# Performance work log

Hardware: AMD Instinct MI355X
Metric: run time of the kernel (lower is better)

The kernel has to match this reference:

```python
import jax, jax.numpy as jnp
import numpy as np

B, C, H, W = 8, 512, 64, 64
C8 = C // 8


def setup_inputs() -> dict:
    key = jax.random.key(0)
    ks = jax.random.split(key, 9)
    s = 1.0 / np.sqrt(C)
    return {
        "view1": jax.random.normal(ks[0], (B, C, H, W), jnp.float32),
        "view2": jax.random.normal(ks[1], (B, C, H, W), jnp.float32),
        "Wq": jax.random.normal(ks[2], (C8, C), jnp.float32) * s,
        "bq": jax.random.normal(ks[3], (C8,), jnp.float32) * 0.01,
        "Wk": jax.random.normal(ks[4], (C8, C), jnp.float32) * s,
        "bk": jax.random.normal(ks[5], (C8,), jnp.float32) * 0.01,
        "Wv": jax.random.normal(ks[6], (C, C), jnp.float32) * s,
        "bv": jax.random.normal(ks[7], (C,), jnp.float32) * 0.01,
        "gamma": jnp.array([0.5], jnp.float32),  # nn.Parameter(zeros(1)) in torch; nonzero here for nontrivial output
    }


def reference(view1, view2, Wq, bq, Wk, bk, Wv, bv, gamma):
    b, c, h, w = view1.shape
    n = h * w
    # 1x1 convs == per-pixel linear over channel dim
    q = jnp.einsum("bchw,oc->bohw", view1, Wq) + bq[None, :, None, None]
    k = jnp.einsum("bchw,oc->bohw", view2, Wk) + bk[None, :, None, None]
    v = jnp.einsum("bchw,oc->bohw", view2, Wv) + bv[None, :, None, None]
    q = q.reshape(b, -1, n).transpose(0, 2, 1)  # (B, N, C/8)
    k = k.reshape(b, -1, n)                      # (B, C/8, N)
    v = v.reshape(b, c, n)                       # (B, C, N)
    # no scaling, matching the original module
    attn = jax.nn.softmax(jnp.einsum("bnd,bdm->bnm", q, k), axis=-1)  # (B, N, N)
    out = jnp.einsum("bcn,bmn->bcm", v, attn).reshape(b, c, h, w)
    return gamma[0] * out + view1
```

## Files before the change

### kernel.cpp

```cpp
#include <hip/hip_runtime.h>

#define NB 8
#define NC 512
#define NPIX 4096
#define LOG2E 1.44269504088896340736f
#define C0TERM 28.853900817779268f

typedef __attribute__((ext_vector_type(4))) float f32x4;
typedef __attribute__((ext_vector_type(8))) short bf16x8;
typedef __attribute__((ext_vector_type(4))) unsigned short u16x4;

static __device__ __forceinline__ short f2bf(float f){
    union { float f; unsigned u; } v; v.f = f;
    unsigned r = v.u + 0x7fffu + ((v.u >> 16) & 1u);
    return (short)(r >> 16);
}

static __device__ __forceinline__ void gload16(const void* g, void* l){
    __builtin_amdgcn_global_load_lds(
        (const __attribute__((address_space(1))) char*)g,
        (__attribute__((address_space(3))) char*)l, 16, 0, 0);
}

#define VW6 asm volatile("s_waitcnt vmcnt(6)" ::: "memory")
#define VW0 asm volatile("s_waitcnt vmcnt(0)" ::: "memory")
#define BAR __builtin_amdgcn_s_barrier()
#define SB0 __builtin_amdgcn_sched_barrier(0)

__global__ void k_wconv(const float* __restrict__ wq, const float* __restrict__ wk,
                        const float* __restrict__ wv,
                        short* __restrict__ wqb, short* __restrict__ wkb,
                        short* __restrict__ wvb){
    int i = blockIdx.x * 256 + threadIdx.x;
    if (i < 64*NC){ wqb[i] = f2bf(wq[i]); wkb[i] = f2bf(wk[i]); }
    if (i < NC*NC){ wvb[i] = f2bf(wv[i]); }
}

__global__ __launch_bounds__(256) void k_projq(const float* __restrict__ X,
                                               const short* __restrict__ W,
                                               const float* __restrict__ bias,
                                               short* __restrict__ out){
    const int b = blockIdx.y;
    const int wv = threadIdx.x >> 6;
    const int lane = threadIdx.x & 63;
    const int g = lane >> 4, c16 = lane & 15;
    const int n0w = blockIdx.x * 64 + wv * 16;
    const float* Xb = X + (size_t)b * NC * NPIX;

    f32x4 acc[4];
#pragma unroll
    for (int f = 0; f < 4; ++f) acc[f] = (f32x4){0.f,0.f,0.f,0.f};

    for (int c0 = 0; c0 < NC; c0 += 32){
        bf16x8 a;
#pragma unroll
        for (int j = 0; j < 8; ++j)
            a[j] = f2bf(Xb[(size_t)(c0 + 8*g + j) * NPIX + n0w + c16]);
#pragma unroll
        for (int f = 0; f < 4; ++f){
            bf16x8 bfr = *(const bf16x8*)(W + (size_t)(f*16 + c16) * NC + c0 + 8*g);
            acc[f] = __builtin_amdgcn_mfma_f32_16x16x32_bf16(a, bfr, acc[f], 0, 0, 0);
        }
    }
#pragma unroll
    for (int f = 0; f < 4; ++f){
        int o = f*16 + c16;
        float bo = bias[o];
#pragma unroll
        for (int i = 0; i < 4; ++i)
            out[((size_t)b*NPIX + n0w + 4*g + i)*64 + o] = f2bf(acc[f][i] + bo);
    }
}

__global__ __launch_bounds__(256) void k_trans(const float* __restrict__ X,
                                               short* __restrict__ Xt){
    __shared__ __align__(16) short T[64][72];
    const int n0 = blockIdx.x * 64;
    const int c0 = blockIdx.y * 64;
    const int b  = blockIdx.z;
    const int t  = threadIdx.x;
    {
        const int cl = t >> 2;
        const int nq = (t & 3) * 16;
        const float* src = X + ((size_t)b*NC + c0 + cl)*NPIX + n0 + nq;
#pragma unroll
        for (int q = 0; q < 4; ++q){
            f32x4 v = *(const f32x4*)(src + q*4);
#pragma unroll
            for (int i = 0; i < 4; ++i)
                T[nq + q*4 + i][cl] = f2bf(v[i]);
        }
    }
    __syncthreads();
    {
        const int n  = t >> 2;
        const int cs = (t & 3) * 16;
        short* dst = Xt + ((size_t)b*NPIX + n0 + n)*NC + c0 + cs;
        *(f32x4*)dst       = *(const f32x4*)&T[n][cs];
        *(f32x4*)(dst + 8) = *(const f32x4*)&T[n][cs + 8];
    }
}

__global__ __launch_bounds__(256) void k_projv(const short* __restrict__ Xt,
                                               const short* __restrict__ W,
                                               const float* __restrict__ bias,
                                               short* __restrict__ vout){
    const int o0 = blockIdx.x * 128;
    const int n0 = blockIdx.y * 128;
    const int b  = blockIdx.z;
    const int wv = threadIdx.x >> 6;
    const int lane = threadIdx.x & 63;
    const int g = lane >> 4, c16 = lane & 15;
    const int wo = wv & 1, wn = wv >> 1;

    const short* Xb = Xt + ((size_t)b*NPIX + n0 + wn*64)*NC;
    const short* Wb = W + (size_t)(o0 + wo*64)*NC;

    f32x4 acc[4][4];
#pragma unroll
    for (int nf = 0; nf < 4; ++nf)
#pragma unroll
        for (int of = 0; of < 4; ++of) acc[nf][of] = (f32x4){0.f,0.f,0.f,0.f};

    for (int c0 = 0; c0 < NC; c0 += 32){
        bf16x8 af[4], bf_[4];
#pragma unroll
        for (int f = 0; f < 4; ++f){
            af[f]  = *(const bf16x8*)(Xb + (size_t)(f*16 + c16)*NC + c0 + 8*g);
            bf_[f] = *(const bf16x8*)(Wb + (size_t)(f*16 + c16)*NC + c0 + 8*g);
        }
#pragma unroll
        for (int nf = 0; nf < 4; ++nf)
#pragma unroll
            for (int of = 0; of < 4; ++of)
                acc[nf][of] = __builtin_amdgcn_mfma_f32_16x16x32_bf16(af[nf], bf_[of], acc[nf][of], 0,0,0);
    }

#pragma unroll
    for (int of = 0; of < 4; ++of){
        int o = o0 + wo*64 + of*16 + c16;
        float bo = bias[o];
#pragma unroll
        for (int nf = 0; nf < 4; ++nf){
            int n = n0 + wn*64 + nf*16 + 4*g;
            u16x4 pk;
#pragma unroll
            for (int i = 0; i < 4; ++i) pk[i] = (unsigned short)f2bf(acc[nf][of][i] + bo);
            *(u16x4*)(vout + ((size_t)b*NC + o)*NPIX + n) = pk;
        }
    }
}

__global__ __launch_bounds__(256) void k_projk(const short* __restrict__ Xt,
                                               const short* __restrict__ W,
                                               const float* __restrict__ bias,
                                               short* __restrict__ kout){
    const int n0 = blockIdx.x * 256;
    const int b  = blockIdx.y;
    const int wv = threadIdx.x >> 6;
    const int lane = threadIdx.x & 63;
    const int g = lane >> 4, c16 = lane & 15;

    const short* Xb = Xt + ((size_t)b*NPIX + n0 + wv*64)*NC;

    f32x4 acc[4][4];
#pragma unroll
    for (int of = 0; of < 4; ++of)
#pragma unroll
        for (int nf = 0; nf < 4; ++nf) acc[of][nf] = (f32x4){0.f,0.f,0.f,0.f};

    for (int c0 = 0; c0 < NC; c0 += 32){
        bf16x8 af[4], bf_[4];
#pragma unroll
        for (int f = 0; f < 4; ++f){
            af[f]  = *(const bf16x8*)(W + (size_t)(f*16 + c16)*NC + c0 + 8*g);
            bf_[f] = *(const bf16x8*)(Xb + (size_t)(f*16 + c16)*NC + c0 + 8*g);
        }
#pragma unroll
        for (int of = 0; of < 4; ++of)
#pragma unroll
            for (int nf = 0; nf < 4; ++nf)
                acc[of][nf] = __builtin_amdgcn_mfma_f32_16x16x32_bf16(af[of], bf_[nf], acc[of][nf], 0,0,0);
    }

#pragma unroll
    for (int nf = 0; nf < 4; ++nf){
        int n = n0 + wv*64 + nf*16 + c16;
#pragma unroll
        for (int of = 0; of < 4; ++of){
            int o = of*16 + 4*g;
            u16x4 pk;
#pragma unroll
            for (int i = 0; i < 4; ++i) pk[i] = (unsigned short)f2bf(acc[of][nf][i] + bias[o+i]);
            *(u16x4*)(kout + ((size_t)b*NPIX + n)*64 + o) = pk;
        }
    }
}

__global__ __launch_bounds__(256) void k_projkv(const float* __restrict__ X,
                                                const short* __restrict__ Wv_,
                                                const float* __restrict__ bv_,
                                                const short* __restrict__ Wk_,
                                                const float* __restrict__ bk_,
                                                short* __restrict__ vout,
                                                short* __restrict__ kout){
    const int b = blockIdx.y;
    const int wv = threadIdx.x >> 6;
    const int lane = threadIdx.x & 63;
    const int g = lane >> 4, c16 = lane & 15;
    const int n0w = blockIdx.x * 32 + (wv & 1) * 16;
    const int oh = wv >> 1;
    const int o0v = oh * 256;
    const int o0k = oh * 32;
    const float* Xb = X + (size_t)b * NC * NPIX;

    f32x4 accv[16], acck[2];
#pragma unroll
    for (int f = 0; f < 16; ++f) accv[f] = (f32x4){0.f,0.f,0.f,0.f};
#pragma unroll
    for (int f = 0; f < 2;  ++f) acck[f] = (f32x4){0.f,0.f,0.f,0.f};

    for (int c0 = 0; c0 < NC; c0 += 32){
        bf16x8 a;
#pragma unroll
        for (int j = 0; j < 8; ++j)
            a[j] = f2bf(Xb[(size_t)(c0 + 8*g + j) * NPIX + n0w + c16]);
#pragma unroll
        for (int f = 0; f < 16; ++f){
            bf16x8 bfr = *(const bf16x8*)(Wv_ + (size_t)(o0v + f*16 + c16) * NC + c0 + 8*g);
            accv[f] = __builtin_amdgcn_mfma_f32_16x16x32_bf16(a, bfr, accv[f], 0, 0, 0);
        }
#pragma unroll
        for (int f = 0; f < 2; ++f){
            bf16x8 bfr = *(const bf16x8*)(Wk_ + (size_t)(o0k + f*16 + c16) * NC + c0 + 8*g);
            acck[f] = __builtin_amdgcn_mfma_f32_16x16x32_bf16(a, bfr, acck[f], 0, 0, 0);
        }
    }
#pragma unroll
    for (int f = 0; f < 16; ++f){
        int o = o0v + f*16 + c16;
        float bo = bv_[o];
        u16x4 pk;
#pragma unroll
        for (int i = 0; i < 4; ++i) pk[i] = (unsigned short)f2bf(accv[f][i] + bo);
        *(u16x4*)(vout + ((size_t)b*NC + o)*NPIX + n0w + 4*g) = pk;
    }
#pragma unroll
    for (int f = 0; f < 2; ++f){
        int o = o0k + f*16 + c16;
        float bo = bk_[o];
#pragma unroll
        for (int i = 0; i < 4; ++i)
            kout[((size_t)b*NPIX + n0w + 4*g + i)*64 + o] = f2bf(acck[f][i] + bo);
    }
}

__global__ __launch_bounds__(256) void k_qk(const short* __restrict__ qb,
                                            const short* __restrict__ kb,
                                            short* __restrict__ P,
                                            float* __restrict__ Lpart,
                                            int b0){
    __shared__ __align__(16) short Pt[64*256];
    const int m0 = blockIdx.x * 64;
    const int n0 = blockIdx.y * 256;
    const int bz = blockIdx.z;
    const int b  = b0 + bz;
    const int wv = threadIdx.x >> 6;
    const int lane = threadIdx.x & 63;
    const int g = lane >> 4, c16 = lane & 15;
    const int nsub = wv * 64;

    bf16x8 qf[4][2];
#pragma unroll
    for (int mf = 0; mf < 4; ++mf)
#pragma unroll
        for (int kk = 0; kk < 2; ++kk)
            qf[mf][kk] = *(const bf16x8*)(qb + ((size_t)b*NPIX + m0 + mf*16 + c16)*64 + kk*32 + 8*g);

    float lsum[4] = {0.f,0.f,0.f,0.f};
    char* Ptb = (char*)Pt;

#pragma unroll
    for (int nf = 0; nf < 4; ++nf){
        bf16x8 kf0 = *(const bf16x8*)(kb + ((size_t)b*NPIX + n0 + nsub + nf*16 + c16)*64 + 8*g);
        bf16x8 kf1 = *(const bf16x8*)(kb + ((size_t)b*NPIX + n0 + nsub + nf*16 + c16)*64 + 32 + 8*g);
#pragma unroll
        for (int mf = 0; mf < 4; ++mf){
            f32x4 s = (f32x4){0.f,0.f,0.f,0.f};
            s = __builtin_amdgcn_mfma_f32_16x16x32_bf16(kf0, qf[mf][0], s, 0,0,0);
            s = __builtin_amdgcn_mfma_f32_16x16x32_bf16(kf1, qf[mf][1], s, 0,0,0);
            u16x4 pk;
#pragma unroll
            for (int i = 0; i < 4; ++i){
                float p = exp2f(fmaf(s[i], LOG2E, -C0TERM));
                lsum[mf] += p;
                pk[i] = (unsigned short)f2bf(p);
            }
            int m = mf*16 + c16;
            int ncol = nsub + nf*16 + 4*g;
            *(u16x4*)(Ptb + m*512 + ((2*ncol) ^ ((m&7)<<4))) = pk;
        }
    }
    __syncthreads();

    {
        char* Pgb = (char*)(P + ((size_t)bz*NPIX + m0)*NPIX + n0);
        const int chunk = threadIdx.x & 31;
        const int row8  = threadIdx.x >> 5;
#pragma unroll
        for (int p = 0; p < 8; ++p){
            int row = p*8 + row8;
            f32x4 v = *(const f32x4*)(Ptb + row*512 + ((chunk*16) ^ ((row&7)<<4)));
            *(f32x4*)(Pgb + (size_t)row*(NPIX*2) + chunk*16) = v;
        }
    }

#pragma unroll
    for (int mf = 0; mf < 4; ++mf){
        lsum[mf] += __shfl_xor(lsum[mf], 16);
        lsum[mf] += __shfl_xor(lsum[mf], 32);
    }
    if (lane < 16){
        size_t base = ((size_t)bz*64 + blockIdx.y*4 + wv)*NPIX + m0 + lane;
#pragma unroll
        for (int mf = 0; mf < 4; ++mf)
            Lpart[base + mf*16] = lsum[mf];
    }
}

__global__ __launch_bounds__(256) void k_lred(const float* __restrict__ Lpart,
                                              const float* __restrict__ gamma,
                                              float* __restrict__ scale){
    int idx = blockIdx.x * 256 + threadIdx.x;
    int bz = idx >> 12, m = idx & 4095;
    float s = 0.f;
    for (int sl = 0; sl < 64; ++sl)
        s += Lpart[((size_t)bz*64 + sl)*NPIX + m];
    scale[idx] = gamma[0] / s;
}

__global__ __launch_bounds__(256) void k_pv(const short* __restrict__ vb,
                                            const short* __restrict__ P,
                                            const float* __restrict__ scale,
                                            const float* __restrict__ view1,
                                            float* __restrict__ out,
                                            int b0){
    __shared__ __align__(16) short At[2][128*64];
    __shared__ __align__(16) short Bt[2][64*64];
    const int p  = blockIdx.x + 4*blockIdx.y;
    const int mt = (p & 7) | ((p >> 5) << 3);
    const int ct = (p >> 3) & 3;
    const int c0 = ct * 128;
    const int m0 = mt * 64;
    const int bz = blockIdx.z;
    const int b  = b0 + bz;
    const int wv = threadIdx.x >> 6;
    const int lane = threadIdx.x & 63;
    const int g = lane >> 4, c16 = lane & 15;
    const int wc = wv & 1, wm = wv >> 1;
    const int lrow = lane >> 3;
    const int srcg = (lane & 7) ^ lrow;
    const int swz  = (c16 & 7) << 4;

    const char* Vg = (const char*)(vb + ((size_t)b*NC + c0)*NPIX);
    const char* Pg = (const char*)(P + ((size_t)bz*NPIX + m0)*NPIX);

    f32x4 acc[4][2];
#pragma unroll
    for (int cf = 0; cf < 4; ++cf)
#pragma unroll
        for (int mf = 0; mf < 2; ++mf) acc[cf][mf] = (f32x4){0.f,0.f,0.f,0.f};

    auto stage = [&](int buf, int t){
        size_t nbyte = (size_t)t * 128;
#pragma unroll
        for (int j = 0; j < 4; ++j){
            int r0 = wv*32 + j*8;
            gload16(Vg + (size_t)(r0 + lrow)*(NPIX*2) + nbyte + srcg*16,
                    (char*)&At[buf][0] + r0*128);
        }
#pragma unroll
        for (int j = 0; j < 2; ++j){
            int r0 = wv*16 + j*8;
            gload16(Pg + (size_t)(r0 + lrow)*(NPIX*2) + nbyte + srcg*16,
                    (char*)&Bt[buf][0] + r0*128);
        }
    };

    auto kstep = [&](int buf){
        const char* A  = (const char*)&At[buf][0];
        const char* Bp = (const char*)&Bt[buf][0];
#pragma unroll
        for (int kk = 0; kk < 2; ++kk){
            bf16x8 af[4], bfm[2];
#pragma unroll
            for (int f = 0; f < 4; ++f)
                af[f]  = *(const bf16x8*)(A  + (wc*64 + f*16 + c16)*128 + ((kk*64 + g*16) ^ swz));
#pragma unroll
            for (int f = 0; f < 2; ++f)
                bfm[f] = *(const bf16x8*)(Bp + (wm*32 + f*16 + c16)*128 + ((kk*64 + g*16) ^ swz));
            __builtin_amdgcn_s_setprio(1);
#pragma unroll
            for (int cf = 0; cf < 4; ++cf)
#pragma unroll
                for (int mf = 0; mf < 2; ++mf)
                    acc[cf][mf] = __builtin_amdgcn_mfma_f32_16x16x32_bf16(af[cf], bfm[mf], acc[cf][mf], 0,0,0);
            __builtin_amdgcn_s_setprio(0);
        }
    };

    stage(0, 0);
    stage(1, 1);

    for (int t2 = 0; t2 < 31; ++t2){
        VW6; BAR; SB0;
        kstep(0);
        BAR;
        stage(0, 2*t2 + 2);
        VW6; BAR; SB0;
        kstep(1);
        BAR;
        stage(1, 2*t2 + 3);
    }
    VW6; BAR; SB0;
    kstep(0);
    VW0; BAR; SB0;
    kstep(1);

    float sc[2];
#pragma unroll
    for (int mf = 0; mf < 2; ++mf)
        sc[mf] = scale[(size_t)bz*NPIX + m0 + wm*32 + mf*16 + c16];
#pragma unroll
    for (int cf = 0; cf < 4; ++cf){
#pragma unroll
        for (int mf = 0; mf < 2; ++mf){
            int m = m0 + wm*32 + mf*16 + c16;
#pragma unroll
            for (int i = 0; i < 4; ++i){
                int c = c0 + wc*64 + cf*16 + 4*g + i;
                size_t idx = ((size_t)b*NC + c)*NPIX + m;
                out[idx] = sc[mf]*acc[cf][mf][i] + view1[idx];
            }
        }
    }
}

__global__ __launch_bounds__(512, 2) void k_attn(const short* __restrict__ qb,
                                                 const short* __restrict__ kb,
                                                 const short* __restrict__ vb,
                                                 const float* __restrict__ view1,
                                                 const float* __restrict__ gamma,
                                                 float* __restrict__ out){
    __shared__ __align__(16) short P[2][64*64];
    __shared__ float Lred[128];

    const int bid = blockIdx.x;
    const int b  = bid & 7;
    const int m0 = (bid >> 3) * 64;
    const int wv = threadIdx.x >> 6;
    const int lane = threadIdx.x & 63;
    const int g = lane >> 4, c16 = lane & 15;
    const int msubA = (wv & 3) * 16;
    const int nhalf = wv >> 2;
    const int c0w = wv * 64;

    const short* qrow = qb + ((size_t)b*NPIX + m0 + msubA + c16)*64 + 8*g;
    bf16x8 qa0 = *(const bf16x8*)qrow;
    bf16x8 qa1 = *(const bf16x8*)(qrow + 32);

    const size_t kbase = (size_t)b * NPIX * 64;
    const int mrow = msubA + c16;
    const int swz = (mrow & 7) << 4;
    float Lacc = 0.f;

    f32x4 acc[4][4];
#pragma unroll
    for (int f = 0; f < 4; ++f)
#pragma unroll
        for (int cf = 0; cf < 4; ++cf) acc[f][cf] = (f32x4){0.f,0.f,0.f,0.f};

    char* Pb0 = (char*)&P[0][0];
    char* Pb1 = (char*)&P[1][0];

    bf16x8 vrA[8], vrB[8], krA[4], krB[4];

    auto loadK = [&](int t, bf16x8 (&kr)[4]){
        const short* kp = kb + kbase + (size_t)(t*64 + nhalf*32 + c16)*64 + 8*g;
        kr[0] = *(const bf16x8*)kp;
        kr[1] = *(const bf16x8*)(kp + 32);
        kr[2] = *(const bf16x8*)(kp + 16*64);
        kr[3] = *(const bf16x8*)(kp + 16*64 + 32);
    };
    auto loadV = [&](int t, bf16x8 (&vr)[8]){
#pragma unroll
        for (int h = 0; h < 2; ++h)
#pragma unroll
            for (int cf = 0; cf < 4; ++cf)
                vr[h*4+cf] = *(const bf16x8*)(vb + ((size_t)b*NC + c0w + cf*16 + c16)*NPIX
                                              + t*64 + h*32 + 8*g);
    };

    auto compA = [&](bf16x8 kA, bf16x8 kB, int fn, char* pb){
        f32x4 s = (f32x4){0.f,0.f,0.f,0.f};
        s = __builtin_amdgcn_mfma_f32_16x16x32_bf16(kA, qa0, s, 0,0,0);
        s = __builtin_amdgcn_mfma_f32_16x16x32_bf16(kB, qa1, s, 0,0,0);
        u16x4 pk;
#pragma unroll
        for (int i = 0; i < 4; ++i){
            float p = exp2f(fmaf(s[i], LOG2E, -C0TERM));
            Lacc += p;
            pk[i] = (unsigned short)f2bf(p);
        }
        int nrel0 = nhalf*32 + fn*16 + 4*g;
        *(u16x4*)(pb + mrow*128 + ((2*nrel0) ^ swz)) = pk;
    };

    auto phaseB = [&](const char* pc, const bf16x8 (&vr)[8]){
#pragma unroll
        for (int h = 0; h < 2; ++h){
            bf16x8 pa[4];
#pragma unroll
            for (int f = 0; f < 4; ++f){
                int row = f*16 + c16;
                pa[f] = *(const bf16x8*)(pc + row*128 + ((h*64 + g*16) ^ ((row&7)<<4)));
            }
#pragma unroll
            for (int cf = 0; cf < 4; ++cf)
#pragma unroll
                for (int f = 0; f < 4; ++f)
                    acc[f][cf] = __builtin_amdgcn_mfma_f32_16x16x32_bf16(pa[f], vr[h*4+cf], acc[f][cf], 0,0,0);
        }
    };

    auto iter = [&](int t, char* bufA, const char* bufB,
                    const bf16x8 (&vcur)[8], bf16x8 (&vnext)[8],
                    const bf16x8 (&kcur)[4], bf16x8 (&knext)[4]){
        loadV(t+1, vnext);
        loadK(t+2 < 64 ? t+2 : 63, knext);
        __builtin_amdgcn_s_setprio(1);
        phaseB(bufB, vcur);
        __builtin_amdgcn_s_setprio(0);
        compA(kcur[0], kcur[1], 0, bufA);
        compA(kcur[2], kcur[3], 1, bufA);
        asm volatile("s_waitcnt lgkmcnt(0)" ::: "memory");
        __builtin_amdgcn_s_barrier();
    };

    loadV(0, vrA);
    loadK(0, krA);
    loadK(1, krB);
    compA(krA[0], krA[1], 0, Pb0);
    compA(krA[2], krA[3], 1, Pb0);
    asm volatile("s_waitcnt lgkmcnt(0)" ::: "memory");
    __builtin_amdgcn_s_barrier();

    for (int t2 = 0; t2 < 31; ++t2){
        iter(2*t2,     Pb1, Pb0, vrA, vrB, krB, krA);
        iter(2*t2 + 1, Pb0, Pb1, vrB, vrA, krA, krB);
    }
    iter(62, Pb1, Pb0, vrA, vrB, krB, krA);
    __builtin_amdgcn_s_setprio(1);
    phaseB(Pb1, vrB);
    __builtin_amdgcn_s_setprio(0);

    Lacc += __shfl_xor(Lacc, 16);
    Lacc += __shfl_xor(Lacc, 32);
    if (lane < 16) Lred[nhalf*64 + msubA + lane] = Lacc;
    __syncthreads();

    float gm = gamma[0];
#pragma unroll
    for (int f = 0; f < 4; ++f){
        float sc[4];
#pragma unroll
        for (int i = 0; i < 4; ++i){
            int r = f*16 + 4*g + i;
            float Ls = Lred[r] + Lred[64 + r];
            sc[i] = gm / Ls;
        }
#pragma unroll
        for (int cf = 0; cf < 4; ++cf){
            int c = c0w + cf*16 + c16;
            size_t base = ((size_t)b*NC + c)*NPIX + m0 + f*16 + 4*g;
            f32x4 v1 = *(const f32x4*)(view1 + base);
            f32x4 r;
#pragma unroll
            for (int i = 0; i < 4; ++i) r[i] = sc[i]*acc[f][cf][i] + v1[i];
            *(f32x4*)(out + base) = r;
        }
    }
}

extern "C" void kernel_launch(void* const* d_in, const int* in_sizes, int n_in,
                              void* d_out, int out_size, void* d_ws, size_t ws_size,
                              hipStream_t stream){
    const float* view1 = (const float*)d_in[0];
    const float* view2 = (const float*)d_in[1];
    const float* Wq    = (const float*)d_in[2];
    const float* bq    = (const float*)d_in[3];
    const float* Wk    = (const float*)d_in[4];
    const float* bk    = (const float*)d_in[5];
    const float* Wv    = (const float*)d_in[6];
    const float* bv    = (const float*)d_in[7];
    const float* gamma = (const float*)d_in[8];
    float* out = (float*)d_out;

    char* ws = (char*)d_ws;
    short* qbuf = (short*)(ws);
    short* kbuf = (short*)(ws + (size_t)4*1024*1024);
    short* vbuf = (short*)(ws + (size_t)8*1024*1024);
    short* wqb  = (short*)(ws + (size_t)40*1024*1024);
    short* wkb  = (short*)(ws + (size_t)40*1024*1024 + 64*1024);
    short* wvb  = (short*)(ws + (size_t)40*1024*1024 + 128*1024);
    float* scl  = (float*)(ws + (size_t)41*1024*1024);
    float* Lpart= (float*)(ws + (size_t)42*1024*1024);
    short* Pbuf = (short*)(ws + (size_t)50*1024*1024);
    short* X2t  = Pbuf;
    short* X1t  = Pbuf + (size_t)16*1024*1024;

    const size_t FIXED = (size_t)50*1024*1024;
    const size_t PPB   = (size_t)NPIX*NPIX*2;
    int avail = 0;
    if (ws_size > FIXED){
        size_t nn = (ws_size - FIXED) / PPB;
        avail = nn > 8 ? 8 : (int)nn;
    }
    int nbc = (avail >= 8) ? 8 : (avail >= 4) ? 4 : (avail >= 2) ? 2 : avail;

    hipLaunchKernelGGL(k_wconv, dim3(1024), dim3(256), 0, stream, Wq, Wk, Wv, wqb, wkb, wvb);

    if (nbc >= 1){
        hipLaunchKernelGGL(k_trans, dim3(64, 8, 8), dim3(256), 0, stream, view2, X2t);
        hipLaunchKernelGGL(k_projv, dim3(4, 32, 8), dim3(256), 0, stream, X2t, wvb, bv, vbuf);
        hipLaunchKernelGGL(k_projk, dim3(16, 8),    dim3(256), 0, stream, X2t, wkb, bk, kbuf);
        if (nbc >= 2){
            hipLaunchKernelGGL(k_trans, dim3(64, 8, 8), dim3(256), 0, stream, view1, X1t);
            hipLaunchKernelGGL(k_projk, dim3(16, 8),    dim3(256), 0, stream, X1t, wqb, bq, qbuf);
        } else {
            hipLaunchKernelGGL(k_projq, dim3(64, 8), dim3(256), 0, stream, view1, wqb, bq, qbuf);
        }
        for (int b0 = 0; b0 < NB; b0 += nbc){
            int nb = (NB - b0 < nbc) ? (NB - b0) : nbc;
            hipLaunchKernelGGL(k_qk,   dim3(64, 16, nb), dim3(256), 0, stream, qbuf, kbuf, Pbuf, Lpart, b0);
            hipLaunchKernelGGL(k_lred, dim3(nb*16),      dim3(256), 0, stream, Lpart, gamma, scl);
            hipLaunchKernelGGL(k_pv,   dim3(4, 64, nb),  dim3(256), 0, stream, vbuf, Pbuf, scl, view1, out, b0);
        }
    } else {
        hipLaunchKernelGGL(k_projq,  dim3(64, 8),  dim3(256), 0, stream, view1, wqb, bq, qbuf);
        hipLaunchKernelGGL(k_projkv, dim3(128, 8), dim3(256), 0, stream, view2, wvb, bv, wkb, bk, vbuf, kbuf);
        hipLaunchKernelGGL(k_attn, dim3(512), dim3(512), 0, stream, qbuf, kbuf, vbuf, view1, gamma, out);
    }
}
```

Measured before the change: 497.7 us.

## Enlarge PV tile to 128x256 with 512 threads and triple-buffered LDS pipeline

The P·V kernel now uses 512-thread blocks that each compute a 128-channel by 256-pixel output tile instead of 128x64. This raises operand reuse, so each P tile is read by fewer blocks and global traffic per MFMA drops. LDS staging becomes a 3-deep ring, with prefetch loads interleaved across the four MFMA sub-steps of each k-tile. The costs are more LDS per block (about 144KB), more barriers per iteration, fewer blocks in the grid, and the loss of the previous swizzled block-order mapping.

```diff
diff --git a/kernel.cpp b/kernel.cpp
--- a/kernel.cpp
+++ b/kernel.cpp
@@ -24,6 +24,7 @@
 
 #define VW6 asm volatile("s_waitcnt vmcnt(6)" ::: "memory")
 #define VW0 asm volatile("s_waitcnt vmcnt(0)" ::: "memory")
+#define LK0 asm volatile("s_waitcnt lgkmcnt(0)" ::: "memory")
 #define BAR __builtin_amdgcn_s_barrier()
 #define SB0 __builtin_amdgcn_sched_barrier(0)
 
@@ -339,25 +340,25 @@
     scale[idx] = gamma[0] / s;
 }
 
-__global__ __launch_bounds__(256) void k_pv(const short* __restrict__ vb,
+__global__ __launch_bounds__(512) void k_pv(const short* __restrict__ vb,
                                             const short* __restrict__ P,
                                             const float* __restrict__ scale,
                                             const float* __restrict__ view1,
                                             float* __restrict__ out,
                                             int b0){
-    __shared__ __align__(16) short At[2][128*64];
-    __shared__ __align__(16) short Bt[2][64*64];
-    const int p  = blockIdx.x + 4*blockIdx.y;
-    const int mt = (p & 7) | ((p >> 5) << 3);
-    const int ct = (p >> 3) & 3;
+    __shared__ __align__(16) short Vt[3][128*64];
+    __shared__ __align__(16) short Pl[3][256*64];
+    const int mt = blockIdx.x;
+    const int ct = blockIdx.y;
     const int c0 = ct * 128;
-    const int m0 = mt * 64;
+    const int m0 = mt * 256;
     const int bz = blockIdx.z;
     const int b  = b0 + bz;
     const int wv = threadIdx.x >> 6;
     const int lane = threadIdx.x & 63;
     const int g = lane >> 4, c16 = lane & 15;
-    const int wc = wv & 1, wm = wv >> 1;
+    const int wm = wv >> 2;
+    const int wc = wv & 3;
     const int lrow = lane >> 3;
     const int srcg = (lane & 7) ^ lrow;
     const int swz  = (c16 & 7) << 4;
@@ -365,82 +366,89 @@
     const char* Vg = (const char*)(vb + ((size_t)b*NC + c0)*NPIX);
     const char* Pg = (const char*)(P + ((size_t)bz*NPIX + m0)*NPIX);
 
-    f32x4 acc[4][2];
-#pragma unroll
-    for (int cf = 0; cf < 4; ++cf)
-#pragma unroll
-        for (int mf = 0; mf < 2; ++mf) acc[cf][mf] = (f32x4){0.f,0.f,0.f,0.f};
-
-    auto stage = [&](int buf, int t){
-        size_t nbyte = (size_t)t * 128;
-#pragma unroll
-        for (int j = 0; j < 4; ++j){
-            int r0 = wv*32 + j*8;
-            gload16(Vg + (size_t)(r0 + lrow)*(NPIX*2) + nbyte + srcg*16,
-                    (char*)&At[buf][0] + r0*128);
-        }
-#pragma unroll
-        for (int j = 0; j < 2; ++j){
-            int r0 = wv*16 + j*8;
-            gload16(Pg + (size_t)(r0 + lrow)*(NPIX*2) + nbyte + srcg*16,
-                    (char*)&Bt[buf][0] + r0*128);
-        }
-    };
-
-    auto kstep = [&](int buf){
-        const char* A  = (const char*)&At[buf][0];
-        const char* Bp = (const char*)&Bt[buf][0];
-#pragma unroll
-        for (int kk = 0; kk < 2; ++kk){
-            bf16x8 af[4], bfm[2];
+    f32x4 acc[8][2];
+#pragma unroll
+    for (int mf = 0; mf < 8; ++mf)
+#pragma unroll
+        for (int cf = 0; cf < 2; ++cf) acc[mf][cf] = (f32x4){0.f,0.f,0.f,0.f};
+
+    auto stageP = [&](int buf, int t, int j){
+        int r0 = wv*32 + j*8;
+        gload16(Pg + (size_t)(r0 + lrow)*(NPIX*2) + (size_t)t*128 + srcg*16,
+                (char*)&Pl[buf][0] + r0*128);
+    };
+    auto stageV = [&](int buf, int t, int j){
+        int r0 = wv*16 + j*8;
+        gload16(Vg + (size_t)(r0 + lrow)*(NPIX*2) + (size_t)t*128 + srcg*16,
+                (char*)&Vt[buf][0] + r0*128);
+    };
+    auto stageAll = [&](int buf, int t){
+#pragma unroll
+        for (int j = 0; j < 4; ++j) stageP(buf, t, j);
+#pragma unroll
+        for (int j = 0; j < 2; ++j) stageV(buf, t, j);
+    };
+
+    stageAll(0, 0);
+    stageAll(1, 1);
+    VW6; BAR; SB0;
+
+    for (int t = 0; t < 64; ++t){
+        const int buf = t % 3;
+        const int nbuf = (t + 2) % 3;
+        const bool prefetch = (t < 62);
+        const char* Vb = (const char*)&Vt[buf][0];
+        const char* Pb = (const char*)&Pl[buf][0];
+#pragma unroll
+        for (int q = 0; q < 4; ++q){
+            const int q64 = q >> 1;
+            const int kk  = q & 1;
+            bf16x8 pf[4], vf[2];
 #pragma unroll
             for (int f = 0; f < 4; ++f)
-                af[f]  = *(const bf16x8*)(A  + (wc*64 + f*16 + c16)*128 + ((kk*64 + g*16) ^ swz));
+                pf[f] = *(const bf16x8*)(Pb + (wm*128 + q64*64 + f*16 + c16)*128
+                                            + ((kk*64 + g*16) ^ swz));
 #pragma unroll
             for (int f = 0; f < 2; ++f)
-                bfm[f] = *(const bf16x8*)(Bp + (wm*32 + f*16 + c16)*128 + ((kk*64 + g*16) ^ swz));
+                vf[f] = *(const bf16x8*)(Vb + (wc*32 + f*16 + c16)*128
+                                            + ((kk*64 + g*16) ^ swz));
+            if (prefetch){
+                if (q == 1){ stageP(nbuf, t+2, 0); stageP(nbuf, t+2, 1); }
+                if (q == 2){ stageP(nbuf, t+2, 2); stageP(nbuf, t+2, 3); }
+                if (q == 3){ stageV(nbuf, t+2, 0); stageV(nbuf, t+2, 1); }
+            }
+            BAR;
+            LK0; SB0;
             __builtin_amdgcn_s_setprio(1);
 #pragma unroll
-            for (int cf = 0; cf < 4; ++cf)
-#pragma unroll
-                for (int mf = 0; mf < 2; ++mf)
-                    acc[cf][mf] = __builtin_amdgcn_mfma_f32_16x16x32_bf16(af[cf], bfm[mf], acc[cf][mf], 0,0,0);
+            for (int f = 0; f < 4; ++f)
+#pragma unroll
+                for (int cf = 0; cf < 2; ++cf)
+                    acc[q64*4 + f][cf] =
+                        __builtin_amdgcn_mfma_f32_16x16x32_bf16(vf[cf], pf[f], acc[q64*4 + f][cf], 0,0,0);
             __builtin_amdgcn_s_setprio(0);
-        }
-    };
-
-    stage(0, 0);
-    stage(1, 1);
-
-    for (int t2 = 0; t2 < 31; ++t2){
-        VW6; BAR; SB0;
-        kstep(0);
-        BAR;
-        stage(0, 2*t2 + 2);
-        VW6; BAR; SB0;
-        kstep(1);
-        BAR;
-        stage(1, 2*t2 + 3);
-    }
-    VW6; BAR; SB0;
-    kstep(0);
-    VW0; BAR; SB0;
-    kstep(1);
-
-    float sc[2];
-#pragma unroll
-    for (int mf = 0; mf < 2; ++mf)
-        sc[mf] = scale[(size_t)bz*NPIX + m0 + wm*32 + mf*16 + c16];
-#pragma unroll
-    for (int cf = 0; cf < 4; ++cf){
-#pragma unroll
-        for (int mf = 0; mf < 2; ++mf){
-            int m = m0 + wm*32 + mf*16 + c16;
+            if (q == 3){
+                if (t < 62){ VW6; }
+                else if (t == 62){ VW0; }
+            }
+            BAR;
+        }
+    }
+
+    float sc[8];
+#pragma unroll
+    for (int mf = 0; mf < 8; ++mf)
+        sc[mf] = scale[(size_t)bz*NPIX + m0 + wm*128 + mf*16 + c16];
+#pragma unroll
+    for (int mf = 0; mf < 8; ++mf){
+        int m = m0 + wm*128 + mf*16 + c16;
+#pragma unroll
+        for (int cf = 0; cf < 2; ++cf){
 #pragma unroll
             for (int i = 0; i < 4; ++i){
-                int c = c0 + wc*64 + cf*16 + 4*g + i;
+                int c = c0 + wc*32 + cf*16 + 4*g + i;
                 size_t idx = ((size_t)b*NC + c)*NPIX + m;
-                out[idx] = sc[mf]*acc[cf][mf][i] + view1[idx];
+                out[idx] = sc[mf]*acc[mf][cf][i] + view1[idx];
             }
         }
     }
@@ -644,7 +652,7 @@
             int nb = (NB - b0 < nbc) ? (NB - b0) : nbc;
             hipLaunchKernelGGL(k_qk,   dim3(64, 16, nb), dim3(256), 0, stream, qbuf, kbuf, Pbuf, Lpart, b0);
             hipLaunchKernelGGL(k_lred, dim3(nb*16),      dim3(256), 0, stream, Lpart, gamma, scl);
-            hipLaunchKernelGGL(k_pv,   dim3(4, 64, nb),  dim3(256), 0, stream, vbuf, Pbuf, scl, view1, out, b0);
+            hipLaunchKernelGGL(k_pv,   dim3(16, 4, nb),  dim3(512), 0, stream, vbuf, Pbuf, scl, view1, out, b0);
         }
     } else {
         hipLaunchKernelGGL(k_projq,  dim3(64, 8),  dim3(256), 0, stream, view1, wqb, bq, qbuf);
```

Measured after the change: 454.2 us. 1.1x faster.
